# Kernel tuning notes

Measured on AMD Instinct MI355X. Metric: run time of the kernel, lower is better.

The kernel has to match this reference:

```python
import jax, jax.numpy as jnp
import numpy as np

HIDDEN = 1024
HEADS = 16
HEAD_DIM = HIDDEN // HEADS
B, S = 2, 2048


def setup_inputs() -> dict:
    key = jax.random.key(0)
    k1, k2, k3 = jax.random.split(key, 3)
    scale_in = 1.0 / np.sqrt(HIDDEN)
    x = jax.random.normal(k1, (B, S, HIDDEN), dtype=jnp.float32)
    wqkv_w = jax.random.normal(k2, (3 * HIDDEN, HIDDEN), dtype=jnp.float32) * scale_in
    wo_w = jax.random.normal(k3, (HIDDEN, HIDDEN), dtype=jnp.float32) * scale_in
    wo_b = jnp.zeros((HIDDEN,), dtype=jnp.float32)
    return {"x": x, "wqkv_w": wqkv_w, "wo_w": wo_w, "wo_b": wo_b}


def reference(x, wqkv_w, wo_w, wo_b):
    b, s, d = x.shape
    h, hd = HEADS, HEAD_DIM
    sm_scale = hd ** (-0.5)
    # QKV projection (torch Linear: x @ W^T), then chunk into q,k,v
    qkv = jnp.einsum('bsd,ed->bse', x, wqkv_w)  # [b, s, 3d]
    q, k, v = jnp.split(qkv, 3, axis=-1)
    # [b, h, s, hd]
    q = q.reshape(b, s, h, hd).transpose(0, 2, 1, 3)
    k = k.reshape(b, s, h, hd).transpose(0, 2, 1, 3)
    v = v.reshape(b, s, h, hd).transpose(0, 2, 1, 3)
    # raw scores, then causal mask (mask applied BEFORE scaling, as in source;
    # -inf * scale == -inf so math matches softmax(score*scale) with mask)
    scores = jnp.einsum('bhqe,bhke->bhqk', q, k)
    causal = jnp.tril(jnp.ones((s, s), dtype=bool))
    scores = jnp.where(causal[None, None, :, :], scores, -jnp.inf)
    weights = jax.nn.softmax(scores * sm_scale, axis=-1)
    # dropout p=0.0 (eval) -> identity
    out = jnp.einsum('bhqk,bhke->bhqe', weights, v)
    out = out.transpose(0, 2, 1, 3).reshape(b, s, h * hd)
    y = jnp.einsum('bsd,ed->bse', out, wo_w) + wo_b
    return (y, k, v)
```

## Files before the change

kernel.cpp:

```cpp
#include <hip/hip_runtime.h>
#include <cstdint>
#include <cstddef>


using bf16x8 = __attribute__((ext_vector_type(8))) __bf16;
using f32x4  = __attribute__((ext_vector_type(4))) float;
using u16    = unsigned short;

#define SOFT_SCALE 0.1803368801111244f

__device__ __forceinline__ u16 f2bf(float f) {
  union { float f; uint32_t u; } a; a.f = f;
  uint32_t r = a.u + 0x7fffu + ((a.u >> 16) & 1u);
  return (u16)(r >> 16);
}

__device__ __forceinline__ bf16x8 ldfrag(const u16* p) {
  return *reinterpret_cast<const bf16x8*>(p);
}

__device__ __forceinline__ void gload_lds16(const void* g, void* l) {
  __builtin_amdgcn_global_load_lds((const __attribute__((address_space(1))) void*)g,
                                   (__attribute__((address_space(3))) void*)l,
                                   16, 0, 0);
}

__device__ __forceinline__ uint32_t cvt_pk_bf16(float a, float b) {
  uint32_t r;
  asm("v_cvt_pk_bf16_f32 %0, %1, %2" : "=v"(r) : "v"(a), "v"(b));
  return r;
}

__global__ void cvt_all(const float* __restrict__ x, const float* __restrict__ wqkv,
                        const float* __restrict__ wo,
                        u16* __restrict__ xb, u16* __restrict__ wqkvb, u16* __restrict__ wob) {
  int i = blockIdx.x * blockDim.x + threadIdx.x;
  int stride = gridDim.x * blockDim.x;
  for (; i < 2097152; i += stride) {
    const float* src; u16* dst; int j;
    if (i < 1048576)      { src = x;    dst = xb;    j = i; }
    else if (i < 1835008) { src = wqkv; dst = wqkvb; j = i - 1048576; }
    else                  { src = wo;   dst = wob;   j = i - 1835008; }
    float4 v = reinterpret_cast<const float4*>(src)[j];
    ushort4 o;
    o.x = f2bf(v.x); o.y = f2bf(v.y); o.z = f2bf(v.z); o.w = f2bf(v.w);
    reinterpret_cast<ushort4*>(dst)[j] = o;
  }
}

__global__ __launch_bounds__(512, 2) void qkv_gemm_kernel(
    const u16* __restrict__ Xb, const u16* __restrict__ Wb,
    u16* __restrict__ Qws, u16* __restrict__ Kws, u16* __restrict__ Vtws,
    float* __restrict__ out) {
  extern __shared__ char smem[];

  const int tid = threadIdx.x, lane = tid & 63, wid = tid >> 6;
  const int wr = wid >> 2, wc = wid & 3;
  const int fq = lane >> 4, fr = lane & 15;

  const int wg = (blockIdx.x & 7) * 24 + (blockIdx.x >> 3);
  const int bm = wg / 12, bn = wg % 12;
  const int m0 = bm * 256, n0 = bn * 256;

  const char* Ab = (const char*)Xb + (size_t)m0 * 2048;
  const char* Bb = (const char*)Wb + (size_t)n0 * 2048;

  f32x4 acc[8][4] = {};

  auto stage = [&](int t, int cc) {
    char* As = smem + cc * 32768;
    char* Bs = smem + 65536 + cc * 32768;
#pragma unroll
    for (int f = 0; f < 4; ++f) {
      int lin = (f * 512 + tid) * 16;
      int row = lin >> 7;
      int col = (lin & 127) ^ ((row & 7) << 4);
      gload_lds16(Ab + (size_t)row * 2048 + t * 128 + col, As + lin);
      gload_lds16(Bb + (size_t)row * 2048 + t * 128 + col, Bs + lin);
    }
  };

  stage(0, 0);
  int cur = 0;
  for (int t = 0; t < 16; ++t) {
    if (t < 15) {
      stage(t + 1, cur ^ 1);
      asm volatile("s_waitcnt vmcnt(8)" ::: "memory");
    } else {
      asm volatile("s_waitcnt vmcnt(0)" ::: "memory");
    }
    __builtin_amdgcn_s_barrier();
    __builtin_amdgcn_sched_barrier(0);

    const char* As = smem + cur * 32768;
    const char* Bs = smem + 65536 + cur * 32768;

#pragma unroll
    for (int ks = 0; ks < 2; ++ks) {
      bf16x8 af[8];
#pragma unroll
      for (int m = 0; m < 8; ++m) {
        int row = wr * 128 + m * 16 + fr;
        int col = (ks * 64 + fq * 16) ^ ((row & 7) << 4);
        af[m] = *(const bf16x8*)(As + row * 128 + col);
      }
#pragma unroll
      for (int nh = 0; nh < 2; ++nh) {
        int row0 = wc * 64 + (nh * 2) * 16 + fr;
        int col0 = (ks * 64 + fq * 16) ^ ((row0 & 7) << 4);
        bf16x8 bf0 = *(const bf16x8*)(Bs + row0 * 128 + col0);
        int row1 = wc * 64 + (nh * 2 + 1) * 16 + fr;
        int col1 = (ks * 64 + fq * 16) ^ ((row1 & 7) << 4);
        bf16x8 bf1 = *(const bf16x8*)(Bs + row1 * 128 + col1);
        __builtin_amdgcn_s_setprio(1);
#pragma unroll
        for (int m = 0; m < 8; ++m) {
          acc[m][nh * 2]     = __builtin_amdgcn_mfma_f32_16x16x32_bf16(af[m], bf0, acc[m][nh * 2], 0, 0, 0);
          acc[m][nh * 2 + 1] = __builtin_amdgcn_mfma_f32_16x16x32_bf16(af[m], bf1, acc[m][nh * 2 + 1], 0, 0, 0);
        }
        __builtin_amdgcn_s_setprio(0);
      }
    }
    asm volatile("s_waitcnt lgkmcnt(0)" ::: "memory");
    __builtin_amdgcn_s_barrier();
    cur ^= 1;
  }

  const int sect = n0 >> 10;
  const int nn0 = (n0 & 1023) + wc * 64;
  const int mbase = m0 + wr * 128;
#pragma unroll
  for (int m = 0; m < 8; ++m)
#pragma unroll
    for (int n = 0; n < 4; ++n) {
      int mB = mbase + m * 16 + fq * 4;
      int ncol = nn0 + n * 16 + fr;
      int b = mB >> 11, s0 = mB & 2047;
      int h = ncol >> 6, hd = ncol & 63;
      size_t base = (((size_t)b * 16 + h) * 2048 + s0) * 64 + hd;
      float v0 = acc[m][n][0], v1 = acc[m][n][1], v2 = acc[m][n][2], v3 = acc[m][n][3];
      if (sect == 0) {
        Qws[base] = f2bf(v0); Qws[base + 64] = f2bf(v1);
        Qws[base + 128] = f2bf(v2); Qws[base + 192] = f2bf(v3);
      } else if (sect == 1) {
        Kws[base] = f2bf(v0); Kws[base + 64] = f2bf(v1);
        Kws[base + 128] = f2bf(v2); Kws[base + 192] = f2bf(v3);
        out[4194304 + base] = v0; out[4194304 + base + 64] = v1;
        out[4194304 + base + 128] = v2; out[4194304 + base + 192] = v3;
      } else {
        out[8388608 + base] = v0; out[8388608 + base + 64] = v1;
        out[8388608 + base + 128] = v2; out[8388608 + base + 192] = v3;
        size_t tt = ((size_t)(b * 16 + h) * 64 + hd) * 2048 + s0;
        ushort4 pk; pk.x = f2bf(v0); pk.y = f2bf(v1); pk.z = f2bf(v2); pk.w = f2bf(v3);
        *reinterpret_cast<ushort4*>(Vtws + tt) = pk;
      }
    }
}

__device__ __forceinline__ void gemm128_core(const u16* __restrict__ A,
                                             const u16* __restrict__ B,
                                             int m0, int n0, int K,
                                             u16* As, u16* Bs, f32x4 acc[4][4]) {
  const int tid  = threadIdx.x;
  const int lane = tid & 63;
  const int wid  = tid >> 6;
  const int wr = wid >> 1, wc = wid & 1;
  const int fq = lane >> 4, fr = lane & 15;

  for (int kb = 0; kb < K; kb += 32) {
#pragma unroll
    for (int j = 0; j < 2; ++j) {
      int lin = (j * 256 + tid) * 16;
      int row = lin >> 6;
      int rb  = lin & 63;
      gload_lds16((const char*)(A + (size_t)(m0 + row) * K + kb) + rb, (char*)As + lin);
      gload_lds16((const char*)(B + (size_t)(n0 + row) * K + kb) + rb, (char*)Bs + lin);
    }
    __syncthreads();

    bf16x8 av[4], bv[4];
#pragma unroll
    for (int i = 0; i < 4; ++i) av[i] = ldfrag(As + (wr * 64 + i * 16 + fr) * 32 + fq * 8);
#pragma unroll
    for (int j = 0; j < 4; ++j) bv[j] = ldfrag(Bs + (wc * 64 + j * 16 + fr) * 32 + fq * 8);
    __builtin_amdgcn_s_setprio(1);
#pragma unroll
    for (int i = 0; i < 4; ++i)
#pragma unroll
      for (int j = 0; j < 4; ++j)
        acc[i][j] = __builtin_amdgcn_mfma_f32_16x16x32_bf16(av[i], bv[j], acc[i][j], 0, 0, 0);
    __builtin_amdgcn_s_setprio(0);
    __syncthreads();
  }
}

__global__ __launch_bounds__(256) void attn_kernel(
    const u16* __restrict__ Qw, const u16* __restrict__ Kw,
    const u16* __restrict__ Vtw, u16* __restrict__ Ow) {
  __shared__ u16 Ks[2][64 * 64];
  __shared__ u16 Vs[2][64 * 64];
  __shared__ u16 Ps[4 * 16 * 64];

  const int tid = threadIdx.x, lane = tid & 63, wid = tid >> 6;
  const int fq = lane >> 4, fr = lane & 15;
  const int bh = blockIdx.x & 31;
  const int qb = 31 - (blockIdx.x >> 5);
  const int b = bh >> 4, h = bh & 15;
  const int q0 = qb * 64;

  const u16* Qbase  = Qw  + (size_t)bh * 2048 * 64;
  const u16* Kbase  = Kw  + (size_t)bh * 2048 * 64;
  const char* VtBase = (const char*)(Vtw + (size_t)bh * 64 * 2048);
  u16* Psw = Ps + wid * 1024;
  char* PswB = (char*)Psw;

#pragma unroll
  for (int f = 0; f < 2; ++f) {
    int lin = (f * 256 + tid) * 16;
    int row = lin >> 7;
    int logical = lin ^ ((row & 7) << 4);
    gload_lds16((const char*)Kbase + logical, (char*)Ks[0] + lin);
    gload_lds16(VtBase + (size_t)row * 4096 + (logical & 127), (char*)Vs[0] + lin);
  }

  const int qrow = q0 + wid * 16 + fr;
  bf16x8 qa0 = ldfrag(Qbase + (size_t)qrow * 64 + fq * 8);
  bf16x8 qa1 = ldfrag(Qbase + (size_t)qrow * 64 + 32 + fq * 8);

  float ssum = 0.f;
  f32x4 accO[4] = {};

  int cur = 0;
  for (int kb = 0; kb <= qb; ++kb) {
    __syncthreads();

    if (kb < qb) {
      const char* kg = (const char*)(Kbase + (size_t)(kb + 1) * 64 * 64);
#pragma unroll
      for (int f = 0; f < 2; ++f) {
        int lin = (f * 256 + tid) * 16;
        int row = lin >> 7;
        int logical = lin ^ ((row & 7) << 4);
        gload_lds16(kg + logical, (char*)Ks[cur ^ 1] + lin);
        gload_lds16(VtBase + (size_t)row * 4096 + (size_t)(kb + 1) * 128 + (logical & 127),
                    (char*)Vs[cur ^ 1] + lin);
      }
    }

    const u16* Kc = Ks[cur];
    const u16* Vc = Vs[cur];

    f32x4 sfr[4];
    __builtin_amdgcn_s_setprio(1);
#pragma unroll
    for (int n = 0; n < 4; ++n) {
      int krow = n * 16 + fr;
      bf16x8 kf0 = ldfrag(Kc + krow * 64 + ((fq * 8)      ^ ((krow & 7) << 3)));
      bf16x8 kf1 = ldfrag(Kc + krow * 64 + ((fq * 8 + 32) ^ ((krow & 7) << 3)));
      f32x4 z = {};
      z = __builtin_amdgcn_mfma_f32_16x16x32_bf16(kf0, qa0, z, 0, 0, 0);
      z = __builtin_amdgcn_mfma_f32_16x16x32_bf16(kf1, qa1, z, 0, 0, 0);
      sfr[n] = z;
    }
    __builtin_amdgcn_s_setprio(0);

#pragma unroll
    for (int n = 0; n < 4; ++n) {
      float p0, p1, p2, p3;
      if (kb < qb) {
        p0 = exp2f(sfr[n][0] * SOFT_SCALE);
        p1 = exp2f(sfr[n][1] * SOFT_SCALE);
        p2 = exp2f(sfr[n][2] * SOFT_SCALE);
        p3 = exp2f(sfr[n][3] * SOFT_SCALE);
      } else {
        int kvg = kb * 64 + n * 16 + fq * 4;
        p0 = (kvg + 0 > qrow) ? 0.f : exp2f(sfr[n][0] * SOFT_SCALE);
        p1 = (kvg + 1 > qrow) ? 0.f : exp2f(sfr[n][1] * SOFT_SCALE);
        p2 = (kvg + 2 > qrow) ? 0.f : exp2f(sfr[n][2] * SOFT_SCALE);
        p3 = (kvg + 3 > qrow) ? 0.f : exp2f(sfr[n][3] * SOFT_SCALE);
      }
      ssum += (p0 + p1) + (p2 + p3);
      uint2 w;
      w.x = cvt_pk_bf16(p0, p1);
      w.y = cvt_pk_bf16(p2, p3);
      *reinterpret_cast<uint2*>(PswB + fr * 128 + ((n * 32 + fq * 8) ^ ((fr & 7) << 4))) = w;
    }

    bf16x8 pa0 = *(const bf16x8*)(PswB + fr * 128 + ((fq * 16)      ^ ((fr & 7) << 4)));
    bf16x8 pa1 = *(const bf16x8*)(PswB + fr * 128 + ((fq * 16 + 64) ^ ((fr & 7) << 4)));
    __builtin_amdgcn_s_setprio(1);
#pragma unroll
    for (int nh = 0; nh < 4; ++nh) {
      int vrow = nh * 16 + fr;
      bf16x8 vb0 = ldfrag(Vc + vrow * 64 + ((fq * 8)      ^ ((vrow & 7) << 3)));
      bf16x8 vb1 = ldfrag(Vc + vrow * 64 + ((fq * 8 + 32) ^ ((vrow & 7) << 3)));
      accO[nh] = __builtin_amdgcn_mfma_f32_16x16x32_bf16(pa0, vb0, accO[nh], 0, 0, 0);
      accO[nh] = __builtin_amdgcn_mfma_f32_16x16x32_bf16(pa1, vb1, accO[nh], 0, 0, 0);
    }
    __builtin_amdgcn_s_setprio(0);
    cur ^= 1;
  }

  ssum += __shfl_xor(ssum, 16);
  ssum += __shfl_xor(ssum, 32);
  float inv = 1.0f / ssum;
  float invq[4];
#pragma unroll
  for (int r = 0; r < 4; ++r) invq[r] = __shfl(inv, fq * 4 + r);

#pragma unroll
  for (int nh = 0; nh < 4; ++nh)
#pragma unroll
    for (int r = 0; r < 4; ++r) {
      float o = accO[nh][r] * invq[r];
      int qr = q0 + wid * 16 + fq * 4 + r;
      Ow[((size_t)b * 2048 + qr) * 1024 + h * 64 + nh * 16 + fr] = f2bf(o);
    }
}

__global__ __launch_bounds__(256) void proj_gemm_kernel(
    const u16* __restrict__ Ob, const u16* __restrict__ Wob,
    const float* __restrict__ bias, float* __restrict__ out) {
  __shared__ u16 As[128 * 32];
  __shared__ u16 Bs[128 * 32];
  const int NB = 8;
  int m0 = (blockIdx.x / NB) * 128, n0 = (blockIdx.x % NB) * 128;
  f32x4 acc[4][4] = {};
  gemm128_core(Ob, Wob, m0, n0, 1024, As, Bs, acc);

  const int lane = threadIdx.x & 63, wid = threadIdx.x >> 6;
  const int wr = wid >> 1, wc = wid & 1, fq = lane >> 4, fr = lane & 15;
#pragma unroll
  for (int i = 0; i < 4; ++i)
#pragma unroll
    for (int j = 0; j < 4; ++j)
#pragma unroll
      for (int r = 0; r < 4; ++r) {
        int m = m0 + wr * 64 + i * 16 + fq * 4 + r;
        int n = n0 + wc * 64 + j * 16 + fr;
        out[(size_t)m * 1024 + n] = acc[i][j][r] + bias[n];
      }
}

extern "C" void kernel_launch(void* const* d_in, const int* in_sizes, int n_in,
                              void* d_out, int out_size, void* d_ws, size_t ws_size,
                              hipStream_t stream) {
  const float* x    = (const float*)d_in[0];
  const float* wqkv = (const float*)d_in[1];
  const float* wo   = (const float*)d_in[2];
  const float* wo_b = (const float*)d_in[3];
  float* out = (float*)d_out;

  u16* xb    = (u16*)d_ws;
  u16* wqkvb = xb    + 4194304;
  u16* wob   = wqkvb + 3145728;
  u16* q_ws  = wob   + 1048576;
  u16* k_ws  = q_ws  + 4194304;
  u16* vt_ws = k_ws  + 4194304;
  u16* o_ws  = vt_ws + 4194304;

  static bool attr_set = false;
  if (!attr_set) {
    hipFuncSetAttribute((const void*)qkv_gemm_kernel,
                        hipFuncAttributeMaxDynamicSharedMemorySize, 131072);
    attr_set = true;
  }

  cvt_all<<<2048, 256, 0, stream>>>(x, wqkv, wo, xb, wqkvb, wob);
  qkv_gemm_kernel<<<192, 512, 131072, stream>>>(xb, wqkvb, q_ws, k_ws, vt_ws, out);
  attn_kernel<<<32 * 32, 256, 0, stream>>>(q_ws, k_ws, vt_ws, o_ws);
  proj_gemm_kernel<<<32 * 8, 256, 0, stream>>>(o_ws, wob, wo_b, out);
}
```

Baseline: 124.5 us.

## Double attention query tile per block and fold softmax scale into Q

Each attention block now handles 128 query rows instead of 64, with every wave owning 32 rows as two 16-row groups. Each staged K/V tile then serves twice as many MFMAs, which halves the global K/V traffic and the number of blocks. The softmax scale is multiplied into Q when it is written in the QKV epilogue, which removes one multiply per score before exp2. In exchange, the grid drops to 512 blocks, register pressure rises, and warps whose rows lie entirely before a tile sit idle on causal diagonal tiles.

```diff
diff --git a/kernel.cpp b/kernel.cpp
--- a/kernel.cpp
+++ b/kernel.cpp
@@ -140,8 +140,10 @@
       size_t base = (((size_t)b * 16 + h) * 2048 + s0) * 64 + hd;
       float v0 = acc[m][n][0], v1 = acc[m][n][1], v2 = acc[m][n][2], v3 = acc[m][n][3];
       if (sect == 0) {
-        Qws[base] = f2bf(v0); Qws[base + 64] = f2bf(v1);
-        Qws[base + 128] = f2bf(v2); Qws[base + 192] = f2bf(v3);
+        Qws[base]       = f2bf(v0 * SOFT_SCALE);
+        Qws[base + 64]  = f2bf(v1 * SOFT_SCALE);
+        Qws[base + 128] = f2bf(v2 * SOFT_SCALE);
+        Qws[base + 192] = f2bf(v3 * SOFT_SCALE);
       } else if (sect == 1) {
         Kws[base] = f2bf(v0); Kws[base + 64] = f2bf(v1);
         Kws[base + 128] = f2bf(v2); Kws[base + 192] = f2bf(v3);
@@ -199,123 +201,146 @@
     const u16* __restrict__ Vtw, u16* __restrict__ Ow) {
   __shared__ u16 Ks[2][64 * 64];
   __shared__ u16 Vs[2][64 * 64];
-  __shared__ u16 Ps[4 * 16 * 64];
+  __shared__ u16 Ps[4 * 32 * 64];
 
   const int tid = threadIdx.x, lane = tid & 63, wid = tid >> 6;
   const int fq = lane >> 4, fr = lane & 15;
   const int bh = blockIdx.x & 31;
-  const int qb = 31 - (blockIdx.x >> 5);
+  const int qb = 15 - (blockIdx.x >> 5);
   const int b = bh >> 4, h = bh & 15;
-  const int q0 = qb * 64;
+  const int q0 = qb * 128;
+  const int qwbase = q0 + wid * 32;
 
   const u16* Qbase  = Qw  + (size_t)bh * 2048 * 64;
   const u16* Kbase  = Kw  + (size_t)bh * 2048 * 64;
   const char* VtBase = (const char*)(Vtw + (size_t)bh * 64 * 2048);
-  u16* Psw = Ps + wid * 1024;
-  char* PswB = (char*)Psw;
-
-#pragma unroll
-  for (int f = 0; f < 2; ++f) {
-    int lin = (f * 256 + tid) * 16;
-    int row = lin >> 7;
-    int logical = lin ^ ((row & 7) << 4);
-    gload_lds16((const char*)Kbase + logical, (char*)Ks[0] + lin);
-    gload_lds16(VtBase + (size_t)row * 4096 + (logical & 127), (char*)Vs[0] + lin);
-  }
-
-  const int qrow = q0 + wid * 16 + fr;
-  bf16x8 qa0 = ldfrag(Qbase + (size_t)qrow * 64 + fq * 8);
-  bf16x8 qa1 = ldfrag(Qbase + (size_t)qrow * 64 + 32 + fq * 8);
-
-  float ssum = 0.f;
-  f32x4 accO[4] = {};
-
+  char* PswB = (char*)(Ps + wid * 2048);
+
+  auto stageKV = [&](int kt, int cc) {
+#pragma unroll
+    for (int f = 0; f < 2; ++f) {
+      int lin = (f * 256 + tid) * 16;
+      int row = lin >> 7;
+      int logical = lin ^ ((row & 7) << 4);
+      gload_lds16((const char*)Kbase + (size_t)kt * 8192 + logical, (char*)Ks[cc] + lin);
+      gload_lds16(VtBase + (size_t)row * 4096 + (size_t)kt * 128 + (logical & 127),
+                  (char*)Vs[cc] + lin);
+    }
+  };
+
+  stageKV(0, 0);
+
+  bf16x8 qa[2][2];
+#pragma unroll
+  for (int qg = 0; qg < 2; ++qg)
+#pragma unroll
+    for (int hh = 0; hh < 2; ++hh)
+      qa[qg][hh] = ldfrag(Qbase + (size_t)(qwbase + qg * 16 + fr) * 64 + hh * 32 + fq * 8);
+
+  float ssum[2] = {0.f, 0.f};
+  f32x4 accO[2][4] = {};
+
+  const int ktiles = 2 * qb + 2;
   int cur = 0;
-  for (int kb = 0; kb <= qb; ++kb) {
+  for (int kt = 0; kt < ktiles; ++kt) {
     __syncthreads();
 
-    if (kb < qb) {
-      const char* kg = (const char*)(Kbase + (size_t)(kb + 1) * 64 * 64);
-#pragma unroll
-      for (int f = 0; f < 2; ++f) {
-        int lin = (f * 256 + tid) * 16;
-        int row = lin >> 7;
-        int logical = lin ^ ((row & 7) << 4);
-        gload_lds16(kg + logical, (char*)Ks[cur ^ 1] + lin);
-        gload_lds16(VtBase + (size_t)row * 4096 + (size_t)(kb + 1) * 128 + (logical & 127),
-                    (char*)Vs[cur ^ 1] + lin);
-      }
-    }
-
-    const u16* Kc = Ks[cur];
-    const u16* Vc = Vs[cur];
-
-    f32x4 sfr[4];
-    __builtin_amdgcn_s_setprio(1);
-#pragma unroll
-    for (int n = 0; n < 4; ++n) {
-      int krow = n * 16 + fr;
-      bf16x8 kf0 = ldfrag(Kc + krow * 64 + ((fq * 8)      ^ ((krow & 7) << 3)));
-      bf16x8 kf1 = ldfrag(Kc + krow * 64 + ((fq * 8 + 32) ^ ((krow & 7) << 3)));
-      f32x4 z = {};
-      z = __builtin_amdgcn_mfma_f32_16x16x32_bf16(kf0, qa0, z, 0, 0, 0);
-      z = __builtin_amdgcn_mfma_f32_16x16x32_bf16(kf1, qa1, z, 0, 0, 0);
-      sfr[n] = z;
-    }
-    __builtin_amdgcn_s_setprio(0);
-
-#pragma unroll
-    for (int n = 0; n < 4; ++n) {
-      float p0, p1, p2, p3;
-      if (kb < qb) {
-        p0 = exp2f(sfr[n][0] * SOFT_SCALE);
-        p1 = exp2f(sfr[n][1] * SOFT_SCALE);
-        p2 = exp2f(sfr[n][2] * SOFT_SCALE);
-        p3 = exp2f(sfr[n][3] * SOFT_SCALE);
-      } else {
-        int kvg = kb * 64 + n * 16 + fq * 4;
-        p0 = (kvg + 0 > qrow) ? 0.f : exp2f(sfr[n][0] * SOFT_SCALE);
-        p1 = (kvg + 1 > qrow) ? 0.f : exp2f(sfr[n][1] * SOFT_SCALE);
-        p2 = (kvg + 2 > qrow) ? 0.f : exp2f(sfr[n][2] * SOFT_SCALE);
-        p3 = (kvg + 3 > qrow) ? 0.f : exp2f(sfr[n][3] * SOFT_SCALE);
-      }
-      ssum += (p0 + p1) + (p2 + p3);
-      uint2 w;
-      w.x = cvt_pk_bf16(p0, p1);
-      w.y = cvt_pk_bf16(p2, p3);
-      *reinterpret_cast<uint2*>(PswB + fr * 128 + ((n * 32 + fq * 8) ^ ((fr & 7) << 4))) = w;
-    }
-
-    bf16x8 pa0 = *(const bf16x8*)(PswB + fr * 128 + ((fq * 16)      ^ ((fr & 7) << 4)));
-    bf16x8 pa1 = *(const bf16x8*)(PswB + fr * 128 + ((fq * 16 + 64) ^ ((fr & 7) << 4)));
-    __builtin_amdgcn_s_setprio(1);
-#pragma unroll
-    for (int nh = 0; nh < 4; ++nh) {
-      int vrow = nh * 16 + fr;
-      bf16x8 vb0 = ldfrag(Vc + vrow * 64 + ((fq * 8)      ^ ((vrow & 7) << 3)));
-      bf16x8 vb1 = ldfrag(Vc + vrow * 64 + ((fq * 8 + 32) ^ ((vrow & 7) << 3)));
-      accO[nh] = __builtin_amdgcn_mfma_f32_16x16x32_bf16(pa0, vb0, accO[nh], 0, 0, 0);
-      accO[nh] = __builtin_amdgcn_mfma_f32_16x16x32_bf16(pa1, vb1, accO[nh], 0, 0, 0);
-    }
-    __builtin_amdgcn_s_setprio(0);
+    if (kt + 1 < ktiles) stageKV(kt + 1, cur ^ 1);
+
+    if (kt * 64 <= qwbase + 31) {
+      const u16* Kc = Ks[cur];
+      const u16* Vc = Vs[cur];
+
+      f32x4 sfr[2][4];
+      __builtin_amdgcn_s_setprio(1);
+#pragma unroll
+      for (int n = 0; n < 4; ++n) {
+        int krow = n * 16 + fr;
+        bf16x8 kf0 = ldfrag(Kc + krow * 64 + ((fq * 8)      ^ ((krow & 7) << 3)));
+        bf16x8 kf1 = ldfrag(Kc + krow * 64 + ((fq * 8 + 32) ^ ((krow & 7) << 3)));
+#pragma unroll
+        for (int qg = 0; qg < 2; ++qg) {
+          f32x4 z = {};
+          z = __builtin_amdgcn_mfma_f32_16x16x32_bf16(kf0, qa[qg][0], z, 0, 0, 0);
+          z = __builtin_amdgcn_mfma_f32_16x16x32_bf16(kf1, qa[qg][1], z, 0, 0, 0);
+          sfr[qg][n] = z;
+        }
+      }
+      __builtin_amdgcn_s_setprio(0);
+
+      const bool diag = (kt >= 2 * qb);
+#pragma unroll
+      for (int qg = 0; qg < 2; ++qg) {
+        int qrow = qwbase + qg * 16 + fr;
+#pragma unroll
+        for (int n = 0; n < 4; ++n) {
+          float p0, p1, p2, p3;
+          if (!diag) {
+            p0 = exp2f(sfr[qg][n][0]);
+            p1 = exp2f(sfr[qg][n][1]);
+            p2 = exp2f(sfr[qg][n][2]);
+            p3 = exp2f(sfr[qg][n][3]);
+          } else {
+            int kvg = kt * 64 + n * 16 + fq * 4;
+            p0 = (kvg + 0 > qrow) ? 0.f : exp2f(sfr[qg][n][0]);
+            p1 = (kvg + 1 > qrow) ? 0.f : exp2f(sfr[qg][n][1]);
+            p2 = (kvg + 2 > qrow) ? 0.f : exp2f(sfr[qg][n][2]);
+            p3 = (kvg + 3 > qrow) ? 0.f : exp2f(sfr[qg][n][3]);
+          }
+          ssum[qg] += (p0 + p1) + (p2 + p3);
+          uint2 w;
+          w.x = cvt_pk_bf16(p0, p1);
+          w.y = cvt_pk_bf16(p2, p3);
+          int prow = qg * 16 + fr;
+          *reinterpret_cast<uint2*>(PswB + prow * 128 + ((n * 32 + fq * 8) ^ ((prow & 7) << 4))) = w;
+        }
+      }
+
+      bf16x8 pa0[2], pa1[2];
+#pragma unroll
+      for (int qg = 0; qg < 2; ++qg) {
+        int prow = qg * 16 + fr;
+        pa0[qg] = *(const bf16x8*)(PswB + prow * 128 + ((fq * 16)      ^ ((prow & 7) << 4)));
+        pa1[qg] = *(const bf16x8*)(PswB + prow * 128 + ((fq * 16 + 64) ^ ((prow & 7) << 4)));
+      }
+      __builtin_amdgcn_s_setprio(1);
+#pragma unroll
+      for (int nh = 0; nh < 4; ++nh) {
+        int vrow = nh * 16 + fr;
+        bf16x8 vb0 = ldfrag(Vc + vrow * 64 + ((fq * 8)      ^ ((vrow & 7) << 3)));
+        bf16x8 vb1 = ldfrag(Vc + vrow * 64 + ((fq * 8 + 32) ^ ((vrow & 7) << 3)));
+#pragma unroll
+        for (int qg = 0; qg < 2; ++qg) {
+          accO[qg][nh] = __builtin_amdgcn_mfma_f32_16x16x32_bf16(pa0[qg], vb0, accO[qg][nh], 0, 0, 0);
+          accO[qg][nh] = __builtin_amdgcn_mfma_f32_16x16x32_bf16(pa1[qg], vb1, accO[qg][nh], 0, 0, 0);
+        }
+      }
+      __builtin_amdgcn_s_setprio(0);
+    }
     cur ^= 1;
   }
 
-  ssum += __shfl_xor(ssum, 16);
-  ssum += __shfl_xor(ssum, 32);
-  float inv = 1.0f / ssum;
-  float invq[4];
-#pragma unroll
-  for (int r = 0; r < 4; ++r) invq[r] = __shfl(inv, fq * 4 + r);
-
-#pragma unroll
-  for (int nh = 0; nh < 4; ++nh)
-#pragma unroll
-    for (int r = 0; r < 4; ++r) {
-      float o = accO[nh][r] * invq[r];
-      int qr = q0 + wid * 16 + fq * 4 + r;
-      Ow[((size_t)b * 2048 + qr) * 1024 + h * 64 + nh * 16 + fr] = f2bf(o);
-    }
+  float invq[2][4];
+#pragma unroll
+  for (int qg = 0; qg < 2; ++qg) {
+    float s = ssum[qg];
+    s += __shfl_xor(s, 16);
+    s += __shfl_xor(s, 32);
+    float inv = 1.0f / s;
+#pragma unroll
+    for (int r = 0; r < 4; ++r) invq[qg][r] = __shfl(inv, fq * 4 + r);
+  }
+
+#pragma unroll
+  for (int qg = 0; qg < 2; ++qg)
+#pragma unroll
+    for (int nh = 0; nh < 4; ++nh)
+#pragma unroll
+      for (int r = 0; r < 4; ++r) {
+        float o = accO[qg][nh][r] * invq[qg][r];
+        int qr = qwbase + qg * 16 + fq * 4 + r;
+        Ow[((size_t)b * 2048 + qr) * 1024 + h * 64 + nh * 16 + fr] = f2bf(o);
+      }
 }
 
 __global__ __launch_bounds__(256) void proj_gemm_kernel(
@@ -368,6 +393,6 @@
 
   cvt_all<<<2048, 256, 0, stream>>>(x, wqkv, wo, xb, wqkvb, wob);
   qkv_gemm_kernel<<<192, 512, 131072, stream>>>(xb, wqkvb, q_ws, k_ws, vt_ws, out);
-  attn_kernel<<<32 * 32, 256, 0, stream>>>(q_ws, k_ws, vt_ws, o_ws);
+  attn_kernel<<<16 * 32, 256, 0, stream>>>(q_ws, k_ws, vt_ws, o_ws);
   proj_gemm_kernel<<<32 * 8, 256, 0, stream>>>(o_ws, wob, wo_b, out);
 }
```

Result: slower. 140.8 us (+13.1%).

## Pass P via permlane swaps instead of LDS, fold softmax scale into Q

Applied to the files above, without the earlier changes.

The attention P tile moves from the S-accumulator layout to the MFMA A-operand layout using v_permlane32/16_swap register shuffles, replacing the per-wave LDS write and read round trip. The softmax scale is folded into Q when the QKV GEMM stores it, which removes a multiply per score element. Launch bounds now ask for 4 blocks per CU, and dropping the P buffer lowers LDS use. The risks are register pressure from the occupancy hint, and the extra bf16 rounding of the scaled Q, which slightly changes the numerics.

```diff
diff --git a/kernel.cpp b/kernel.cpp
--- a/kernel.cpp
+++ b/kernel.cpp
@@ -140,8 +140,10 @@
       size_t base = (((size_t)b * 16 + h) * 2048 + s0) * 64 + hd;
       float v0 = acc[m][n][0], v1 = acc[m][n][1], v2 = acc[m][n][2], v3 = acc[m][n][3];
       if (sect == 0) {
-        Qws[base] = f2bf(v0); Qws[base + 64] = f2bf(v1);
-        Qws[base + 128] = f2bf(v2); Qws[base + 192] = f2bf(v3);
+        Qws[base]       = f2bf(v0 * SOFT_SCALE);
+        Qws[base + 64]  = f2bf(v1 * SOFT_SCALE);
+        Qws[base + 128] = f2bf(v2 * SOFT_SCALE);
+        Qws[base + 192] = f2bf(v3 * SOFT_SCALE);
       } else if (sect == 1) {
         Kws[base] = f2bf(v0); Kws[base + 64] = f2bf(v1);
         Kws[base + 128] = f2bf(v2); Kws[base + 192] = f2bf(v3);
@@ -194,12 +196,11 @@
   }
 }
 
-__global__ __launch_bounds__(256) void attn_kernel(
+__global__ __launch_bounds__(256, 4) void attn_kernel(
     const u16* __restrict__ Qw, const u16* __restrict__ Kw,
     const u16* __restrict__ Vtw, u16* __restrict__ Ow) {
   __shared__ u16 Ks[2][64 * 64];
   __shared__ u16 Vs[2][64 * 64];
-  __shared__ u16 Ps[4 * 16 * 64];
 
   const int tid = threadIdx.x, lane = tid & 63, wid = tid >> 6;
   const int fq = lane >> 4, fr = lane & 15;
@@ -211,8 +212,6 @@
   const u16* Qbase  = Qw  + (size_t)bh * 2048 * 64;
   const u16* Kbase  = Kw  + (size_t)bh * 2048 * 64;
   const char* VtBase = (const char*)(Vtw + (size_t)bh * 64 * 2048);
-  u16* Psw = Ps + wid * 1024;
-  char* PswB = (char*)Psw;
 
 #pragma unroll
   for (int f = 0; f < 2; ++f) {
@@ -264,38 +263,48 @@
     }
     __builtin_amdgcn_s_setprio(0);
 
+    uint32_t W[4][2];
 #pragma unroll
     for (int n = 0; n < 4; ++n) {
       float p0, p1, p2, p3;
       if (kb < qb) {
-        p0 = exp2f(sfr[n][0] * SOFT_SCALE);
-        p1 = exp2f(sfr[n][1] * SOFT_SCALE);
-        p2 = exp2f(sfr[n][2] * SOFT_SCALE);
-        p3 = exp2f(sfr[n][3] * SOFT_SCALE);
+        p0 = exp2f(sfr[n][0]);
+        p1 = exp2f(sfr[n][1]);
+        p2 = exp2f(sfr[n][2]);
+        p3 = exp2f(sfr[n][3]);
       } else {
         int kvg = kb * 64 + n * 16 + fq * 4;
-        p0 = (kvg + 0 > qrow) ? 0.f : exp2f(sfr[n][0] * SOFT_SCALE);
-        p1 = (kvg + 1 > qrow) ? 0.f : exp2f(sfr[n][1] * SOFT_SCALE);
-        p2 = (kvg + 2 > qrow) ? 0.f : exp2f(sfr[n][2] * SOFT_SCALE);
-        p3 = (kvg + 3 > qrow) ? 0.f : exp2f(sfr[n][3] * SOFT_SCALE);
+        p0 = (kvg + 0 > qrow) ? 0.f : exp2f(sfr[n][0]);
+        p1 = (kvg + 1 > qrow) ? 0.f : exp2f(sfr[n][1]);
+        p2 = (kvg + 2 > qrow) ? 0.f : exp2f(sfr[n][2]);
+        p3 = (kvg + 3 > qrow) ? 0.f : exp2f(sfr[n][3]);
       }
       ssum += (p0 + p1) + (p2 + p3);
-      uint2 w;
-      w.x = cvt_pk_bf16(p0, p1);
-      w.y = cvt_pk_bf16(p2, p3);
-      *reinterpret_cast<uint2*>(PswB + fr * 128 + ((n * 32 + fq * 8) ^ ((fr & 7) << 4))) = w;
-    }
-
-    bf16x8 pa0 = *(const bf16x8*)(PswB + fr * 128 + ((fq * 16)      ^ ((fr & 7) << 4)));
-    bf16x8 pa1 = *(const bf16x8*)(PswB + fr * 128 + ((fq * 16 + 64) ^ ((fr & 7) << 4)));
+      W[n][0] = cvt_pk_bf16(p0, p1);
+      W[n][1] = cvt_pk_bf16(p2, p3);
+    }
+
+    union { uint32_t u[4]; bf16x8 v; } pa0u, pa1u;
+#pragma unroll
+    for (int hh = 0; hh < 2; ++hh) {
+      uint32_t a0 = W[0][hh], b0 = W[1][hh];
+      asm("v_permlane32_swap_b32 %0, %1" : "+v"(a0), "+v"(b0));
+      asm("v_permlane16_swap_b32 %0, %1" : "+v"(a0), "+v"(b0));
+      pa0u.u[hh] = a0; pa0u.u[2 + hh] = b0;
+      uint32_t a1 = W[2][hh], b1 = W[3][hh];
+      asm("v_permlane32_swap_b32 %0, %1" : "+v"(a1), "+v"(b1));
+      asm("v_permlane16_swap_b32 %0, %1" : "+v"(a1), "+v"(b1));
+      pa1u.u[hh] = a1; pa1u.u[2 + hh] = b1;
+    }
+
     __builtin_amdgcn_s_setprio(1);
 #pragma unroll
     for (int nh = 0; nh < 4; ++nh) {
       int vrow = nh * 16 + fr;
       bf16x8 vb0 = ldfrag(Vc + vrow * 64 + ((fq * 8)      ^ ((vrow & 7) << 3)));
       bf16x8 vb1 = ldfrag(Vc + vrow * 64 + ((fq * 8 + 32) ^ ((vrow & 7) << 3)));
-      accO[nh] = __builtin_amdgcn_mfma_f32_16x16x32_bf16(pa0, vb0, accO[nh], 0, 0, 0);
-      accO[nh] = __builtin_amdgcn_mfma_f32_16x16x32_bf16(pa1, vb1, accO[nh], 0, 0, 0);
+      accO[nh] = __builtin_amdgcn_mfma_f32_16x16x32_bf16(pa0u.v, vb0, accO[nh], 0, 0, 0);
+      accO[nh] = __builtin_amdgcn_mfma_f32_16x16x32_bf16(pa1u.v, vb1, accO[nh], 0, 0, 0);
     }
     __builtin_amdgcn_s_setprio(0);
     cur ^= 1;
```

Result: faster. 119.1 us (-4.4%).
